# Kernel tuning notes

Hardware: AMD Instinct MI355X
Metric: run time of the kernel (lower is better)

The kernel has to match this reference:

```python
import jax, jax.numpy as jnp
from jax import lax
import numpy as np

LOGZERO = -1e10  # matches the repo's `logzero` sentinel


def setup_inputs() -> dict:
    key = jax.random.key(0)
    k1, k2, k3, k4 = jax.random.split(key, 4)
    bs, xmax, vocab, ymax = 32, 1024, 1000, 128
    # CTC log-probabilities (ctc_generator output is log_softmax in the repo)
    ctc_out = jax.nn.log_softmax(
        jax.random.normal(k1, (bs, xmax, vocab), jnp.float32), axis=-1)
    src_size = jax.random.randint(k2, (bs,), xmax // 2, xmax + 1)
    src_mask = (jnp.arange(xmax)[None, :] < src_size[:, None])[:, None, :]  # [bs,1,xmax] bool
    ys = jax.random.randint(k3, (bs, ymax), 1, vocab)   # non-blank labels
    ylens = jax.random.randint(k4, (bs,), ymax // 2, ymax + 1)
    return {"ctc_out": ctc_out, "src_mask": src_mask, "src_size": src_size,
            "ys": ys, "ylens": ylens, "blank": 0}


def reference(ctc_out, src_mask, src_size, ys, ylens, blank):
    bs, xmax, vocab = ctc_out.shape
    ymax = ys.shape[1]
    L = 2 * ymax + 1  # blank-interleaved path length

    # mask invalid frames to logzero (masked_fill in torch)
    lp = jnp.where(src_mask.transpose(0, 2, 1), ctc_out, LOGZERO)  # [bs,xmax,vocab]

    # blank-interleaved path: [blank, y1, blank, y2, ..., blank]
    path = jnp.full((bs, L), blank, dtype=ys.dtype).at[:, 1::2].set(ys)
    path_lens = 2 * ylens + 1

    # log-probs gathered along the path: [xmax, bs, L] (time-major for scan)
    lp_path = jnp.take_along_axis(
        lp, jnp.broadcast_to(path[:, None, :], (bs, xmax, L)), axis=2)
    lp_path = lp_path.transpose(1, 0, 2)

    same_tr = path[:, :-2] == path[:, 2:]                 # [bs, L-2]
    idx = jnp.arange(L)
    outside = idx[None, :] >= path_lens[:, None]          # [bs, L]

    alpha0 = jnp.full((bs, L), LOGZERO, jnp.float32).at[:, 0].set(0.0)

    def step(alpha, lp_t):
        m0 = alpha
        m1 = jnp.concatenate([jnp.full((bs, 1), LOGZERO, alpha.dtype), alpha[:, :-1]], axis=1)
        m2 = jnp.concatenate([jnp.full((bs, 2), LOGZERO, alpha.dtype),
                              jnp.where(same_tr, LOGZERO, alpha[:, :-2])], axis=1)
        mat = jnp.stack([m0, m1, m2])                     # [3, bs, L]
        max_prob = jnp.max(mat, axis=0)
        arg = jnp.argmax(mat, axis=0)
        bp_t = idx[None, :] - arg                          # back-pointer (path position)
        max_prob = jnp.where(outside, LOGZERO, max_prob)
        alpha_new = max_prob + lp_t
        return alpha_new, (alpha_new, bp_t)

    _, (alpha_hist, bp) = lax.scan(step, alpha0, lp_path)  # [xmax,bs,L] each
    alpha_full = jnp.concatenate([alpha0[None], alpha_hist], axis=0)  # [xmax+1,bs,L]

    b_idx = jnp.arange(bs)
    alpha_at = alpha_full[src_size, b_idx]                 # [bs, L] alpha at t = src_size
    s1 = alpha_at[b_idx, path_lens - 1]
    s2 = alpha_at[b_idx, path_lens - 2]
    start = jnp.where(s1 > s2, path_lens - 1, path_lens - 2)
    score = jnp.maximum(s1, s2)                            # best alignment log-prob per utt

    # vectorized backtrace over all batches (reverse scan over time)
    def back_step(carry, t):
        tt = jnp.minimum(t + 1, xmax - 1)
        prev = bp[tt, b_idx, carry]                        # bp[b, t+1, state_{t+1}]
        val = jnp.where(t == src_size - 1, start,
                        jnp.where(t < src_size - 1, prev, 0))
        return val, val

    ts = jnp.arange(xmax - 1, -1, -1)
    _, states_rev = lax.scan(back_step, jnp.zeros((bs,), start.dtype), ts)
    states = states_rev[::-1].T                            # [bs, xmax] path positions

    aligned = jnp.take_along_axis(path, states, axis=1)    # [bs, xmax] tokens
    shift = jnp.concatenate([jnp.zeros((bs, 1), aligned.dtype), aligned[:, :-1]], axis=1)
    aligned = jnp.where(aligned == shift, 0, aligned)      # collapse repeats to 0
    shift2 = jnp.concatenate([jnp.zeros((bs, 1), aligned.dtype), aligned[:, :-1]], axis=1)

    csum = jnp.cumsum((shift2 != blank).astype(jnp.int32), axis=1)  # [bs, xmax]
    tm = csum[:, None, :] == jnp.arange(ymax + 1)[None, :, None]    # [bs, ymax+1, xmax]
    last = tm[:, -1, :] & src_mask[:, 0, :]
    last = last.at[b_idx, src_size - 1].set(True)
    tm = tm.at[:, -1, :].set(last)
    trigger_mask = tm & src_mask                           # & x_mask from FaNat.forward

    return score, trigger_mask, ylens + 1
```

## Files before the change

kernel.cpp:

```cpp
#include <hip/hip_runtime.h>
#include <stdint.h>

#define LOGZERO (-1e10f)

static constexpr int BS    = 32;
static constexpr int XMAX  = 1024;
static constexpr int VOCAB = 1000;
static constexpr int YMAX  = 128;
static constexpr int NROWS = YMAX + 1;
static constexpr int CH    = 8;
static constexpr int NPROD = 8;
static constexpr int NWAVES = 1 + NPROD;
static constexpr int NPAIR = XMAX / 2;

__global__ __launch_bounds__(64 * NWAVES) void k_viterbi(
    const float* __restrict__ ctc, const int* __restrict__ src_size,
    const int* __restrict__ ys, const int* __restrict__ ylens,
    const int* __restrict__ blankp, int* __restrict__ csum_ws,
    float* __restrict__ out)
{
    __shared__ float buf[2][CH][256];
    __shared__ unsigned char  bpb[XMAX * 64];
    __shared__ unsigned char  g4pack[XMAX / CH];
    __shared__ unsigned short bp2[NPAIR * 64];
    __shared__ unsigned char  bp2_256[NPAIR];
    __shared__ unsigned short st_lds[XMAX];
    __shared__ int ysl[YMAX];

    const int b    = blockIdx.x;
    const int tid  = threadIdx.x;
    const int wid  = tid >> 6;
    const int lane = tid & 63;
    const int ss   = src_size[b];
    const int yl   = ylens[b];
    const int bv   = blankp[0];
    const int plen = 2 * yl + 1;
    const float LZ = LOGZERO;

    for (int j = tid; j < YMAX; j += 64 * NWAVES) ysl[j] = ys[b * YMAX + j];
    for (int t = tid; t < XMAX; t += 64 * NWAVES) st_lds[t] = 0;
    __syncthreads();

    const int nchunk = (ss + CH - 1) / CH;
    const float* baseg = ctc + (size_t)b * XMAX * VOCAB;

    int start = 0;

    if (wid == 0) {
        const int tokA = ysl[2 * lane];
        const int tokB = ysl[2 * lane + 1];
        const bool al1 = (lane > 0) && (tokA != ysl[2 * lane - 1]);
        const bool al3 = (tokB != tokA);
        const bool o0 = (4 * lane     >= plen);
        const bool o1 = (4 * lane + 1 >= plen);
        const bool o2 = (4 * lane + 2 >= plen);
        const bool o3 = (4 * lane + 3 >= plen);
        const bool o4 = (256 >= plen);
        const int rotidx = (lane + 63) & 63;

        float a0 = (lane == 0) ? 0.0f : LZ;
        float a1 = LZ, a2 = LZ, a3 = LZ, a4 = LZ;
        float rotp = __shfl(a3, rotidx);

        for (int c = 0; c < nchunk; ++c) {
            __builtin_amdgcn_s_barrier();
            asm volatile("" ::: "memory");
            __builtin_amdgcn_sched_barrier(0);
            const int cb = c & 1;
            float4 q[CH];
            #pragma unroll
            for (int r = 0; r < CH; ++r)
                q[r] = *reinterpret_cast<const float4*>(&buf[cb][r][lane * 4]);
            unsigned int g4acc = 0;
            #pragma unroll
            for (int r = 0; r < CH; ++r) {
                const int t = c * CH + r;
                if (t < ss) {
                    float m3 = a3; int g3 = 0;
                    if (a2 > m3) { m3 = a2; g3 = 1; }
                    float sk3 = al3 ? a1 : LZ;
                    if (sk3 > m3) { m3 = sk3; g3 = 2; }
                    float a3n = (o3 ? LZ : m3) + q[r].w;
                    float rot = rotp;
                    rotp = __shfl(a3n, rotidx);
                    float p3 = (lane == 0) ? LZ : rot;
                    float m0 = a0; int g0 = 0; if (p3 > m0) { m0 = p3; g0 = 1; }
                    float m1 = a1; int g1 = 0; if (a0 > m1) { m1 = a0; g1 = 1; }
                    float sk1 = al1 ? p3 : LZ;  if (sk1 > m1) { m1 = sk1; g1 = 2; }
                    float m2 = a2; int g2 = 0; if (a1 > m2) { m2 = a1; g2 = 1; }
                    float m4 = a4; int g4 = 0; if (rot > m4) { m4 = rot; g4 = 1; }
                    a0 = (o0 ? LZ : m0) + q[r].x;
                    a1 = (o1 ? LZ : m1) + q[r].y;
                    a2 = (o2 ? LZ : m2) + q[r].z;
                    a3 = a3n;
                    a4 = (o4 ? LZ : m4) + q[r].x;
                    g4acc |= (unsigned)g4 << r;
                    bpb[t * 64 + lane] =
                        (unsigned char)(g0 | (g1 << 2) | (g2 << 4) | (g3 << 6));
                }
            }
            if (lane == 0) g4pack[c] = (unsigned char)g4acc;
        }

        auto getA = [&](int idx) -> float {
            if (idx == 256) return __shfl(a4, 0);
            int k = idx & 3;
            float pick = (k == 0) ? a0 : (k == 1) ? a1 : (k == 2) ? a2 : a3;
            return __shfl(pick, idx >> 2);
        };
        const float s1v = getA(plen - 1), s2v = getA(plen - 2);
        const float score = (s1v > s2v) ? s1v : s2v;
        start = (s1v > s2v) ? (plen - 1) : (plen - 2);
        if (lane == 0) {
            out[b] = score;
            out[32 + (size_t)BS * NROWS * XMAX + b] = (float)(yl + 1);
        }
    } else {
        const int pr = wid - 1;
        const int tokA = ysl[2 * lane];
        const int tokB = ysl[2 * lane + 1];
        int t0 = pr; if (t0 >= ss) t0 = ss - 1;
        const float* r0 = baseg + (size_t)t0 * VOCAB;
        float vb0 = r0[bv], va0 = r0[tokA], vc0 = r0[tokB];
        int t1 = CH + pr; if (t1 >= ss) t1 = ss - 1;
        const float* r1 = baseg + (size_t)t1 * VOCAB;
        float vb1 = r1[bv], va1 = r1[tokA], vc1 = r1[tokB];
        for (int c = 0; c < nchunk; ++c) {
            if (c & 1) {
                *reinterpret_cast<float4*>(&buf[1][pr][lane * 4]) =
                    make_float4(vb1, va1, vb1, vc1);
                int tn = (c + 2) * CH + pr; if (tn >= ss) tn = ss - 1;
                const float* r = baseg + (size_t)tn * VOCAB;
                vb1 = r[bv]; va1 = r[tokA]; vc1 = r[tokB];
            } else {
                *reinterpret_cast<float4*>(&buf[0][pr][lane * 4]) =
                    make_float4(vb0, va0, vb0, vc0);
                int tn = (c + 2) * CH + pr; if (tn >= ss) tn = ss - 1;
                const float* r = baseg + (size_t)tn * VOCAB;
                vb0 = r[bv]; va0 = r[tokA]; vc0 = r[tokB];
            }
            asm volatile("s_waitcnt lgkmcnt(0)" ::: "memory");
            __builtin_amdgcn_s_barrier();
        }
    }
    __syncthreads();

    const int pmax = (ss - 1) >> 1;
    for (int p = 1 + wid; p <= pmax; p += NWAVES) {
        int oOdd  = bpb[(2 * p + 1) * 64 + lane];
        int oEven = bpb[(2 * p) * 64 + lane];
        int uEven = (lane > 0) ? bpb[(2 * p) * 64 + lane - 1] : 0;
        int evenWin = uEven | (oEven << 8);
        unsigned int acc = 0;
        #pragma unroll
        for (int k = 0; k < 4; ++k) {
            int a1v = (oOdd >> (2 * k)) & 3;
            int sh  = 2 * k - 2 * a1v + 8;
            int a2v = (evenWin >> sh) & 3;
            acc |= (unsigned)(a1v | (a2v << 2)) << (4 * k);
        }
        bp2[p * 64 + lane] = (unsigned short)acc;
        const int tOdd = 2 * p + 1, tEven = 2 * p;
        int a16 = (g4pack[tOdd >> 3] >> (tOdd & 7)) & 1;
        int a26 = (a16 == 0) ? ((g4pack[tEven >> 3] >> (tEven & 7)) & 1)
                             : ((bpb[tEven * 64 + 63] >> 6) & 3);
        if (lane == 0) bp2_256[p] = (unsigned char)(a16 | (a26 << 2));
    }
    __syncthreads();

    if (tid == 0) {
        int s = start, tc = ss - 1;
        st_lds[tc] = (unsigned short)s;
        if ((tc & 1) == 0 && tc >= 1) {
            int arg;
            if (s == 256) arg = (g4pack[tc >> 3] >> (tc & 7)) & 1;
            else arg = (bpb[tc * 64 + (s >> 2)] >> ((s & 3) * 2)) & 3;
            s -= arg; --tc; st_lds[tc] = (unsigned short)s;
        }
        while (tc > 1) {
            int n;
            if (s == 256) n = bp2_256[tc >> 1];
            else n = (bp2[(tc >> 1) * 64 + (s >> 2)] >> ((s & 3) * 4)) & 0xF;
            int sA = s - (n & 3);
            int sB = sA - (n >> 2);
            st_lds[tc - 1] = (unsigned short)sA;
            st_lds[tc - 2] = (unsigned short)sB;
            s = sB; tc -= 2;
        }
        if (tc == 1) {
            int arg;
            if (s == 256) arg = (g4pack[0] >> 1) & 1;
            else arg = (bpb[64 + (s >> 2)] >> ((s & 3) * 2)) & 3;
            s -= arg; st_lds[0] = (unsigned short)s;
        }
    }
    __syncthreads();

    if (wid == 0) {
        auto tok_lds = [&](int stv) -> int { return (stv & 1) ? ysl[stv >> 1] : bv; };
        const int t0c = lane * 16;
        int prev_raw = (t0c == 0) ? 0 : tok_lds(st_lds[t0c - 1]);
        int cnt = 0;
        int csl[16];
        #pragma unroll
        for (int i = 0; i < 16; ++i) {
            int raw = tok_lds(st_lds[t0c + i]);
            int ac = (raw == prev_raw) ? 0 : raw;
            prev_raw = raw;
            csl[i] = cnt;
            cnt += (ac != bv) ? 1 : 0;
        }
        int v = cnt;
        #pragma unroll
        for (int off = 1; off < 64; off <<= 1) {
            int u = __shfl_up(v, off);
            if (lane >= off) v += u;
        }
        const int base_c = v - cnt;
        int* co = csum_ws + b * XMAX + t0c;
        #pragma unroll
        for (int i = 0; i < 16; ++i) co[i] = base_c + csl[i];
    }
}

__global__ __launch_bounds__(256) void k_mask(
    const int* __restrict__ csum_ws, const int* __restrict__ src_size,
    float* __restrict__ out)
{
    int bj = blockIdx.x;
    int b = bj / NROWS, j = bj - b * NROWS;
    int ss = src_size[b];
    const int* cs = csum_ws + b * XMAX;
    float* orow = out + 32 + (size_t)bj * XMAX;
    int t = threadIdx.x * 4;
    float4 v;
    float* vp = &v.x;
    #pragma unroll
    for (int i = 0; i < 4; ++i) {
        int tt = t + i;
        int c = cs[tt];
        bool in = tt < ss;
        bool val;
        if (j < YMAX) val = (c == j) && in;
        else          val = ((c == YMAX) || (tt == ss - 1)) && in;
        vp[i] = val ? 1.0f : 0.0f;
    }
    *(float4*)(orow + t) = v;
}

extern "C" void kernel_launch(void* const* d_in, const int* in_sizes, int n_in,
                              void* d_out, int out_size, void* d_ws, size_t ws_size,
                              hipStream_t stream) {
    const float* ctc      = (const float*)d_in[0];
    const int*   src_size = (const int*)d_in[2];
    const int*   ys       = (const int*)d_in[3];
    const int*   ylens    = (const int*)d_in[4];
    const int*   blankp   = (const int*)d_in[5];
    float* out = (float*)d_out;
    int*   csum_ws = (int*)d_ws;

    k_viterbi<<<BS, 64 * NWAVES, 0, stream>>>(ctc, src_size, ys, ylens, blankp,
                                              csum_ws, out);
    k_mask<<<BS * NROWS, 256, 0, stream>>>(csum_ws, src_size, out);
}
```

Measured before the change: 363.0 us.

## Pre-gather path log-probs in a parallel kernel before the Viterbi pass

Adds a k_gather kernel, launched with many blocks, that scatter-reads the blank and label log-probs for every frame into a dense, time-major workspace of float4 rows. The 32-block Viterbi kernel then streams these rows with coalesced vector loads instead of doing random 4-byte gathers from the large vocab tensor. This moves the latency-bound gather off the serial recursion's critical path. In exchange it needs an extra 32 MB workspace write and read plus one more kernel launch, and it falls back to the old path if the workspace is too small.

```diff
diff --git a/kernel.cpp b/kernel.cpp
--- a/kernel.cpp
+++ b/kernel.cpp
@@ -12,9 +12,41 @@
 static constexpr int NPROD = 8;
 static constexpr int NWAVES = 1 + NPROD;
 static constexpr int NPAIR = XMAX / 2;
-
+static constexpr size_t LPWS_BYTES = (size_t)BS * XMAX * 256 * 4;
+
+__global__ __launch_bounds__(256) void k_gather(
+    const float* __restrict__ ctc, const int* __restrict__ src_size,
+    const int* __restrict__ ys, const int* __restrict__ blankp,
+    float* __restrict__ lp_ws)
+{
+    const int blk  = blockIdx.x;
+    const int b    = blk >> 4;
+    const int seg  = blk & 15;
+    const int wid  = threadIdx.x >> 6;
+    const int lane = threadIdx.x & 63;
+    const int ss   = src_size[b];
+    const int bv   = blankp[0];
+    const int tokA = ys[b * YMAX + 2 * lane];
+    const int tokB = ys[b * YMAX + 2 * lane + 1];
+    const float* baseg = ctc + (size_t)b * XMAX * VOCAB;
+    float* basew = lp_ws + (size_t)b * XMAX * 256 + lane * 4;
+    const int t0 = seg * 64 + wid * 16;
+    #pragma unroll 4
+    for (int r = 0; r < 16; ++r) {
+        const int t = t0 + r;
+        if (t < ss) {
+            const float* rp = baseg + (size_t)t * VOCAB;
+            float vb = rp[bv], va = rp[tokA], vc = rp[tokB];
+            *reinterpret_cast<float4*>(basew + (size_t)t * 256) =
+                make_float4(vb, va, vb, vc);
+        }
+    }
+}
+
+template<bool STAGED>
 __global__ __launch_bounds__(64 * NWAVES) void k_viterbi(
-    const float* __restrict__ ctc, const int* __restrict__ src_size,
+    const float* __restrict__ ctc, const float* __restrict__ lp_ws,
+    const int* __restrict__ src_size,
     const int* __restrict__ ys, const int* __restrict__ ylens,
     const int* __restrict__ blankp, int* __restrict__ csum_ws,
     float* __restrict__ out)
@@ -115,6 +147,24 @@
             out[b] = score;
             out[32 + (size_t)BS * NROWS * XMAX + b] = (float)(yl + 1);
         }
+    } else if (STAGED) {
+        const int pr = wid - 1;
+        const float* basew = lp_ws + (size_t)b * XMAX * 256 + lane * 4;
+        float4 v0 = *reinterpret_cast<const float4*>(basew + (size_t)pr * 256);
+        float4 v1 = *reinterpret_cast<const float4*>(basew + (size_t)(CH + pr) * 256);
+        for (int c = 0; c < nchunk; ++c) {
+            if (c & 1) {
+                *reinterpret_cast<float4*>(&buf[1][pr][lane * 4]) = v1;
+                int tn = (c + 2) * CH + pr; if (tn > XMAX - 1) tn = XMAX - 1;
+                v1 = *reinterpret_cast<const float4*>(basew + (size_t)tn * 256);
+            } else {
+                *reinterpret_cast<float4*>(&buf[0][pr][lane * 4]) = v0;
+                int tn = (c + 2) * CH + pr; if (tn > XMAX - 1) tn = XMAX - 1;
+                v0 = *reinterpret_cast<const float4*>(basew + (size_t)tn * 256);
+            }
+            asm volatile("s_waitcnt lgkmcnt(0)" ::: "memory");
+            __builtin_amdgcn_s_barrier();
+        }
     } else {
         const int pr = wid - 1;
         const int tokA = ysl[2 * lane];
@@ -257,9 +307,19 @@
     const int*   ylens    = (const int*)d_in[4];
     const int*   blankp   = (const int*)d_in[5];
     float* out = (float*)d_out;
-    int*   csum_ws = (int*)d_ws;
-
-    k_viterbi<<<BS, 64 * NWAVES, 0, stream>>>(ctc, src_size, ys, ylens, blankp,
-                                              csum_ws, out);
-    k_mask<<<BS * NROWS, 256, 0, stream>>>(csum_ws, src_size, out);
+
+    const size_t need = LPWS_BYTES + (size_t)BS * XMAX * sizeof(int);
+    if (ws_size >= need) {
+        float* lp_ws   = (float*)d_ws;
+        int*   csum_ws = (int*)((char*)d_ws + LPWS_BYTES);
+        k_gather<<<BS * 16, 256, 0, stream>>>(ctc, src_size, ys, blankp, lp_ws);
+        k_viterbi<true><<<BS, 64 * NWAVES, 0, stream>>>(
+            ctc, lp_ws, src_size, ys, ylens, blankp, csum_ws, out);
+        k_mask<<<BS * NROWS, 256, 0, stream>>>(csum_ws, src_size, out);
+    } else {
+        int* csum_ws = (int*)d_ws;
+        k_viterbi<false><<<BS, 64 * NWAVES, 0, stream>>>(
+            ctc, nullptr, src_size, ys, ylens, blankp, csum_ws, out);
+        k_mask<<<BS * NROWS, 256, 0, stream>>>(csum_ws, src_size, out);
+    }
 }
```

Measured after the change: 393.5 us. 1.08x slower.
